# Performance work log

Measured on AMD Instinct MI355X. Metric: run time of the kernel, lower is better.

Reference implementation:

```python
import jax, jax.numpy as jnp
import numpy as np

N_EMBD = 1024
N_HEAD = 16


def setup_inputs() -> dict:
    key = jax.random.key(0)
    ks = jax.random.split(key, 5)
    C = N_EMBD
    x = jax.random.normal(ks[0], (4, 2048, C), dtype=jnp.float32)
    # linear params, scaled like torch default init (~U(-1/sqrt(C),1/sqrt(C)))
    s = 1.0 / np.sqrt(C)
    W_attn = jax.random.uniform(ks[1], (C, 3 * C), jnp.float32, -s, s)
    b_attn = jax.random.uniform(ks[2], (3 * C,), jnp.float32, -s, s)
    W_proj = jax.random.uniform(ks[3], (C, C), jnp.float32, -s, s)
    b_proj = jax.random.uniform(ks[4], (C,), jnp.float32, -s, s)
    return {"x": x, "W_attn": W_attn, "b_attn": b_attn, "W_proj": W_proj, "b_proj": b_proj}


def reference(x, W_attn, b_attn, W_proj, b_proj):
    B, T, C = x.shape
    H = N_HEAD
    D = C // H
    qkv = x @ W_attn + b_attn                      # [B,T,3C]
    q, k, v = jnp.split(qkv, 3, axis=-1)
    # [B,T,C] -> [B,H,T,D]
    q = q.reshape(B, T, H, D).transpose(0, 2, 1, 3)
    k = k.reshape(B, T, H, D).transpose(0, 2, 1, 3)
    v = v.reshape(B, T, H, D).transpose(0, 2, 1, 3)
    scale = 1.0 / np.sqrt(D).astype(np.float32)
    att = jnp.einsum('bhqd,bhkd->bhqk', q, k) * scale  # [B,H,T,T]
    causal = jnp.tril(jnp.ones((T, T), dtype=bool))
    att = jnp.where(causal[None, None], att, -jnp.inf)
    att = jax.nn.softmax(att, axis=-1)
    y = jnp.einsum('bhqk,bhkd->bhqd', att, v)      # [B,H,T,D]
    y = y.transpose(0, 2, 1, 3).reshape(B, T, C)
    return y @ W_proj + b_proj
```

## Files before the change

### kernel.cpp

```cpp
#include <hip/hip_runtime.h>
#include <hip/hip_bf16.h>
#include <math.h>


typedef __bf16 bf16x8 __attribute__((ext_vector_type(8)));
typedef float f32x4 __attribute__((ext_vector_type(4)));
typedef float f32x16 __attribute__((ext_vector_type(16)));

__device__ __forceinline__ f32x4 mfma16(bf16x8 a, bf16x8 b, f32x4 c) {
    return __builtin_amdgcn_mfma_f32_16x16x32_bf16(a, b, c, 0, 0, 0);
}
__device__ __forceinline__ f32x16 mfma32(bf16x8 a, bf16x8 b, f32x16 c) {
    return __builtin_amdgcn_mfma_f32_32x32x16_bf16(a, b, c, 0, 0, 0);
}

#define GLOBAL_AS __attribute__((address_space(1)))
#define LDS_AS __attribute__((address_space(3)))

__device__ __forceinline__ void async_copy16(const __hip_bfloat16* g, __hip_bfloat16* l) {
    __builtin_amdgcn_global_load_lds((const GLOBAL_AS uint32_t*)g, (LDS_AS uint32_t*)l, 16, 0, 0);
}

__device__ __forceinline__ uint32_t cvtpk(float lo, float hi) {
    uint32_t r;
    asm("v_cvt_pk_bf16_f32 %0, %1, %2" : "=v"(r) : "v"(lo), "v"(hi));
    return r;
}

#define QSCL 0.18033688011112042f

__global__ __launch_bounds__(256) void prep_kernel(
    const float* __restrict__ x, __hip_bfloat16* __restrict__ xb,
    const float* __restrict__ Wa, __hip_bfloat16* __restrict__ WaT,
    const float* __restrict__ Wp, __hip_bfloat16* __restrict__ WpT) {
    int bid = blockIdx.x;
    if (bid < 4096) {
        int i = (bid * 256 + threadIdx.x) * 8;
        union { __hip_bfloat16 h[8]; uint4 v; } tmp;
#pragma unroll
        for (int j = 0; j < 8; ++j) tmp.h[j] = __float2bfloat16(x[i + j]);
        *reinterpret_cast<uint4*>(xb + i) = tmp.v;
        return;
    }
    __shared__ float tile[32][33];
    const float* in;
    __hip_bfloat16* out;
    int R, Cc, tx_blocks, tb;
    if (bid < 4096 + 3072) {
        tb = bid - 4096; in = Wa; out = WaT; R = 1024; Cc = 3072; tx_blocks = 96;
    } else {
        tb = bid - 4096 - 3072; in = Wp; out = WpT; R = 1024; Cc = 1024; tx_blocks = 32;
    }
    int c0 = (tb % tx_blocks) * 32, r0 = (tb / tx_blocks) * 32;
    int tx = threadIdx.x & 31, ty = threadIdx.x >> 5;
#pragma unroll
    for (int i = 0; i < 4; ++i) {
        int r = r0 + ty + i * 8;
        tile[ty + i * 8][tx] = in[(size_t)r * Cc + c0 + tx];
    }
    __syncthreads();
#pragma unroll
    for (int i = 0; i < 4; ++i) {
        int c = c0 + ty + i * 8;
        out[(size_t)c * R + r0 + tx] = __float2bfloat16(tile[tx][ty + i * 8]);
    }
}

#define GEMM128_BODY(A_, Bt_, K_)                                                       \
    __shared__ __hip_bfloat16 As[128 * 32];                                             \
    __shared__ __hip_bfloat16 Bs[128 * 32];                                             \
    const int tid = threadIdx.x;                                                        \
    const int w = tid >> 6;                                                             \
    const int lr = tid & 15, lh = (tid & 63) >> 4;                                      \
    const int wr = w >> 1, wc = w & 1;                                                  \
    f32x4 zero = {0.f, 0.f, 0.f, 0.f};                                                  \
    f32x4 acc[4][4];                                                                    \
    _Pragma("unroll") for (int i = 0; i < 4; ++i)                                       \
        _Pragma("unroll") for (int j = 0; j < 4; ++j) acc[i][j] = zero;                 \
    for (int k0 = 0; k0 < (K_); k0 += 32) {                                             \
        _Pragma("unroll") for (int i = 0; i < 2; ++i) {                                 \
            int t = i * 256 + tid;                                                      \
            async_copy16((A_) + (size_t)(m0 + (t >> 2)) * (K_) + k0 + (t & 3) * 8,      \
                         As + (size_t)(i * 256 + w * 64) * 8);                          \
            async_copy16((Bt_) + (size_t)(n0 + (t >> 2)) * (K_) + k0 + (t & 3) * 8,     \
                         Bs + (size_t)(i * 256 + w * 64) * 8);                          \
        }                                                                               \
        __syncthreads();                                                                \
        bf16x8 af[4], bf[4];                                                            \
        _Pragma("unroll") for (int mf = 0; mf < 4; ++mf)                                \
            af[mf] = *reinterpret_cast<const bf16x8*>(                                  \
                &As[(wr * 64 + mf * 16 + lr) * 32 + lh * 8]);                           \
        _Pragma("unroll") for (int nf = 0; nf < 4; ++nf)                                \
            bf[nf] = *reinterpret_cast<const bf16x8*>(                                  \
                &Bs[(wc * 64 + nf * 16 + lr) * 32 + lh * 8]);                           \
        _Pragma("unroll") for (int mf = 0; mf < 4; ++mf)                                \
            _Pragma("unroll") for (int nf = 0; nf < 4; ++nf)                            \
                acc[mf][nf] = mfma16(af[mf], bf[nf], acc[mf][nf]);                      \
        __syncthreads();                                                                \
    }

__global__ __launch_bounds__(256) void gemm_qkv_kernel(
    const __hip_bfloat16* __restrict__ A, const __hip_bfloat16* __restrict__ Bt,
    const float* __restrict__ bias,
    __hip_bfloat16* __restrict__ qd, __hip_bfloat16* __restrict__ kd,
    __hip_bfloat16* __restrict__ vtd) {
    const int K = 1024;
    const int m0 = blockIdx.x * 128;
    const int n0 = blockIdx.y * 128;
    GEMM128_BODY(A, Bt, K)

    const int region = n0 >> 10;
#pragma unroll
    for (int mf = 0; mf < 4; ++mf) {
#pragma unroll
        for (int nf = 0; nf < 4; ++nf) {
            int n = n0 + wc * 64 + nf * 16 + lr;
            float bv = bias[n];
            int mbase = m0 + wr * 64 + mf * 16 + 4 * lh;
            int bb = mbase >> 11;
            int t = mbase & 2047;
            int c = n & 1023, hh = c >> 6, dd = c & 63;
            if (region == 2) {
                union { __hip_bfloat16 h[4]; uint2 v; } pk;
#pragma unroll
                for (int r = 0; r < 4; ++r) pk.h[r] = __float2bfloat16(acc[mf][nf][r] + bv);
                *reinterpret_cast<uint2*>(
                    &vtd[(((size_t)bb * 16 + hh) * 64 + dd) * 2048 + t]) = pk.v;
            } else if (region == 0) {
#pragma unroll
                for (int r = 0; r < 4; ++r)
                    qd[(((size_t)bb * 16 + hh) * 2048 + t + r) * 64 + dd] =
                        __float2bfloat16((acc[mf][nf][r] + bv) * QSCL);
            } else {
#pragma unroll
                for (int r = 0; r < 4; ++r)
                    kd[(((size_t)bb * 16 + hh) * 2048 + t + r) * 64 + dd] =
                        __float2bfloat16(acc[mf][nf][r] + bv);
            }
        }
    }
}

__global__ __launch_bounds__(256) void gemm_proj_kernel(
    const __hip_bfloat16* __restrict__ A, const __hip_bfloat16* __restrict__ Bt,
    const float* __restrict__ bias, float* __restrict__ out) {
    const int K = 1024, N = 1024;
    const int m0 = blockIdx.x * 128;
    const int n0 = blockIdx.y * 128;
    GEMM128_BODY(A, Bt, K)

#pragma unroll
    for (int nf = 0; nf < 4; ++nf) {
        int n = n0 + wc * 64 + nf * 16 + lr;
        float bv = bias[n];
#pragma unroll
        for (int mf = 0; mf < 4; ++mf) {
            int mbase = m0 + wr * 64 + mf * 16 + 4 * lh;
#pragma unroll
            for (int r = 0; r < 4; ++r)
                out[(size_t)(mbase + r) * N + n] = acc[mf][nf][r] + bv;
        }
    }
}

__global__ __launch_bounds__(512) void attn_kernel(
    const __hip_bfloat16* __restrict__ q, const __hip_bfloat16* __restrict__ k,
    const __hip_bfloat16* __restrict__ vt, __hip_bfloat16* __restrict__ y) {
    const int T = 2048, D = 64, C = 1024;
    const float THR = 8.0f;

    int wid = ((int)blockIdx.x & 7) * 64 + ((int)blockIdx.x >> 3);
    int bh = wid >> 3;
    int qr = wid & 7;
    int q256 = (wid & 32) ? qr : 7 - qr;
    int b = bh >> 4, h = bh & 15;
    int tid = threadIdx.x;
    int w = tid >> 6, l = tid & 63;
    int ql = l & 31, hi = l >> 5;

    __shared__ __hip_bfloat16 Ks[64 * 64];
    __shared__ __hip_bfloat16 Vs[64 * 64];
    __shared__ __hip_bfloat16 Pt[8][32][36];

    const int q0 = q256 * 256 + w * 32;
    const __hip_bfloat16* kbh = k + (size_t)bh * T * D;
    const __hip_bfloat16* vbh = vt + (size_t)bh * D * T;

    bf16x8 qf[4];
#pragma unroll
    for (int c = 0; c < 4; ++c)
        qf[c] = *reinterpret_cast<const bf16x8*>(
            q + ((size_t)bh * T + q0 + ql) * D + c * 16 + hi * 8);

    f32x16 o0 = {}, o1 = {};
    float m = -INFINITY, lp = 0.f;

    const int lastSub = q0 >> 5;
    const int nt64 = 4 * q256 + 4;

    for (int t64 = 0; t64 < nt64; ++t64) {
        __syncthreads();
        {
            int slot = tid;
            int row = slot >> 3;
            int fold = ((row & 7) ^ (row >> 3)) & 7;
            int colb = ((slot & 7) * 16) ^ (fold << 4);
            async_copy16(kbh + (size_t)(t64 * 64 + row) * 64 + (colb >> 1),
                         Ks + (size_t)(w * 64) * 8);
            async_copy16(vbh + (size_t)row * T + t64 * 64 + (colb >> 1),
                         Vs + (size_t)(w * 64) * 8);
        }
        __syncthreads();

#pragma unroll
        for (int sub = 0; sub < 2; ++sub) {
            const int is = t64 * 2 + sub;
            if (is > lastSub) break;
            bf16x8 kf[4];
            {
                int krow = sub * 32 + ql;
                int kfold = ((krow & 7) ^ (krow >> 3)) & 7;
                const char* KsB = reinterpret_cast<const char*>(Ks) + krow * 128;
#pragma unroll
                for (int c = 0; c < 4; ++c)
                    kf[c] = *reinterpret_cast<const bf16x8*>(
                        KsB + ((c * 32 + hi * 16) ^ (kfold << 4)));
            }

            __builtin_amdgcn_s_setprio(1);
            f32x16 s = {};
            s = mfma32(kf[0], qf[0], s);
            s = mfma32(kf[1], qf[1], s);
            s = mfma32(kf[2], qf[2], s);
            s = mfma32(kf[3], qf[3], s);
            __builtin_amdgcn_s_setprio(0);

            bf16x8 vf[2][2];
#pragma unroll
            for (int dblk = 0; dblk < 2; ++dblk) {
                int vrow = dblk * 32 + ql;
                int vfold = ((vrow & 7) ^ (vrow >> 3)) & 7;
                const char* VsB = reinterpret_cast<const char*>(Vs) + vrow * 128;
#pragma unroll
                for (int sl = 0; sl < 2; ++sl)
                    vf[dblk][sl] = *reinterpret_cast<const bf16x8*>(
                        VsB + ((sub * 64 + sl * 32 + hi * 16) ^ (vfold << 4)));
            }

            if (is == lastSub) {
#pragma unroll
                for (int r = 0; r < 16; ++r) {
                    int kvrow = (r & 3) + 8 * (r >> 2) + 4 * hi;
                    if (kvrow > ql) s[r] = -INFINITY;
                }
            }

            float mx;
            {
                float a = fmaxf(fmaxf(s[0], s[1]), s[2]);
                float bq = fmaxf(fmaxf(s[3], s[4]), s[5]);
                float c = fmaxf(fmaxf(s[6], s[7]), s[8]);
                float d = fmaxf(fmaxf(s[9], s[10]), s[11]);
                float e = fmaxf(fmaxf(s[12], s[13]), s[14]);
                mx = fmaxf(fmaxf(fmaxf(a, bq), fmaxf(c, d)), fmaxf(e, s[15]));
            }
            mx = fmaxf(mx, __shfl_xor(mx, 32));

            if (!__all(mx - m <= THR)) {
                float mnew = fmaxf(m, mx);
                float al = __builtin_amdgcn_exp2f(m - mnew);
                m = mnew;
                lp *= al;
#pragma unroll
                for (int r = 0; r < 16; ++r) { o0[r] *= al; o1[r] *= al; }
            }

#pragma unroll
            for (int r = 0; r < 16; ++r) s[r] = __builtin_amdgcn_exp2f(s[r] - m);

            lp += ((s[0] + s[1]) + (s[2] + s[3])) + ((s[4] + s[5]) + (s[6] + s[7])) +
                  (((s[8] + s[9]) + (s[10] + s[11])) + ((s[12] + s[13]) + (s[14] + s[15])));

            {
                uint2 w0, w1, w2, w3;
                w0.x = cvtpk(s[0], s[1]);   w0.y = cvtpk(s[2], s[3]);
                w1.x = cvtpk(s[4], s[5]);   w1.y = cvtpk(s[6], s[7]);
                w2.x = cvtpk(s[8], s[9]);   w2.y = cvtpk(s[10], s[11]);
                w3.x = cvtpk(s[12], s[13]); w3.y = cvtpk(s[14], s[15]);
                *reinterpret_cast<uint2*>(&Pt[w][ql][4 * hi])      = w0;
                *reinterpret_cast<uint2*>(&Pt[w][ql][8 + 4 * hi])  = w1;
                *reinterpret_cast<uint2*>(&Pt[w][ql][16 + 4 * hi]) = w2;
                *reinterpret_cast<uint2*>(&Pt[w][ql][24 + 4 * hi]) = w3;
            }

            union { uint32_t u[4]; bf16x8 v; } pa0, pa1;
            {
                uint2 r0 = *reinterpret_cast<const uint2*>(&Pt[w][ql][8 * hi]);
                uint2 r1 = *reinterpret_cast<const uint2*>(&Pt[w][ql][8 * hi + 4]);
                uint2 r2 = *reinterpret_cast<const uint2*>(&Pt[w][ql][16 + 8 * hi]);
                uint2 r3 = *reinterpret_cast<const uint2*>(&Pt[w][ql][16 + 8 * hi + 4]);
                pa0.u[0] = r0.x; pa0.u[1] = r0.y; pa0.u[2] = r1.x; pa0.u[3] = r1.y;
                pa1.u[0] = r2.x; pa1.u[1] = r2.y; pa1.u[2] = r3.x; pa1.u[3] = r3.y;
            }

            __builtin_amdgcn_s_setprio(1);
            o0 = mfma32(vf[0][0], pa0.v, o0);
            o0 = mfma32(vf[0][1], pa1.v, o0);
            o1 = mfma32(vf[1][0], pa0.v, o1);
            o1 = mfma32(vf[1][1], pa1.v, o1);
            __builtin_amdgcn_s_setprio(0);
        }
    }

    lp += __shfl_xor(lp, 32);
    float inv = 1.0f / lp;

    __hip_bfloat16* yq = y + ((size_t)b * T + q0 + ql) * C + h * 64;
#pragma unroll
    for (int dblk = 0; dblk < 2; ++dblk) {
#pragma unroll
        for (int g = 0; g < 4; ++g) {
            union { __hip_bfloat16 h4[4]; uint2 v; } pkk;
#pragma unroll
            for (int r = 0; r < 4; ++r) {
                float val = (dblk ? o1[g * 4 + r] : o0[g * 4 + r]) * inv;
                pkk.h4[r] = __float2bfloat16(val);
            }
            *reinterpret_cast<uint2*>(yq + dblk * 32 + g * 8 + hi * 4) = pkk.v;
        }
    }
}

extern "C" void kernel_launch(void* const* d_in, const int* in_sizes, int n_in,
                              void* d_out, int out_size, void* d_ws, size_t ws_size,
                              hipStream_t stream) {
    const float* x      = (const float*)d_in[0];
    const float* W_attn = (const float*)d_in[1];
    const float* b_attn = (const float*)d_in[2];
    const float* W_proj = (const float*)d_in[3];
    const float* b_proj = (const float*)d_in[4];
    float* out = (float*)d_out;

    __hip_bfloat16* wsb = reinterpret_cast<__hip_bfloat16*>(d_ws);
    __hip_bfloat16* xb  = wsb;
    __hip_bfloat16* WaT = xb + (size_t)8192 * 1024;
    __hip_bfloat16* WpT = WaT + (size_t)3072 * 1024;
    __hip_bfloat16* qd  = WpT + (size_t)1024 * 1024;
    __hip_bfloat16* kd  = qd + (size_t)64 * 2048 * 64;
    __hip_bfloat16* vtd = kd + (size_t)64 * 2048 * 64;
    __hip_bfloat16* ya  = vtd + (size_t)64 * 2048 * 64;

    prep_kernel<<<4096 + 3072 + 1024, 256, 0, stream>>>(x, xb, W_attn, WaT, W_proj, WpT);
    gemm_qkv_kernel<<<dim3(64, 24), 256, 0, stream>>>(xb, WaT, b_attn, qd, kd, vtd);
    attn_kernel<<<512, 512, 0, stream>>>(qd, kd, vtd, ya);
    gemm_proj_kernel<<<dim3(64, 8), 256, 0, stream>>>(ya, WpT, b_proj, out);
}
```

Baseline: 168.9 us.

## Rewrite QKV GEMM as 256x256 double-buffered pipelined tile with swizzled LDS

The QKV projection GEMM moves from 128x128 tiles with 256 threads and a load-sync-compute loop to 256x256 tiles with 512 threads. K-step 64 tiles are double-buffered in LDS, and async global-to-LDS copies for the next stage are interleaved across four MFMA phases using explicit vmcnt waits, barriers and setprio. The LDS layout uses an XOR swizzle to avoid bank conflicts. The aim is to hide load latency and raise data reuse per tile. In exchange it uses 128KB of LDS per block and higher register pressure, and the grid is smaller at 384 blocks.

```diff
diff --git a/kernel.cpp b/kernel.cpp
--- a/kernel.cpp
+++ b/kernel.cpp
@@ -99,42 +99,118 @@
         __syncthreads();                                                                \
     }
 
-__global__ __launch_bounds__(256) void gemm_qkv_kernel(
+#define QKV_PHASE(d_, MF0_, STAGE_STMT, WAIT_STMT)                                      \
+    {                                                                                   \
+        bf16x8 a00 = readA(d_, (MF0_), 0), a01 = readA(d_, (MF0_), 1);                  \
+        bf16x8 a10 = readA(d_, (MF0_) + 1, 0), a11 = readA(d_, (MF0_) + 1, 1);          \
+        STAGE_STMT;                                                                     \
+        asm volatile("s_waitcnt lgkmcnt(0)" ::: "memory");                              \
+        __builtin_amdgcn_sched_barrier(0);                                              \
+        __builtin_amdgcn_s_setprio(1);                                                  \
+        _Pragma("unroll") for (int nf = 0; nf < 4; ++nf) {                              \
+            acc[(MF0_)][nf]     = mfma16(a00, bfr[nf][0], acc[(MF0_)][nf]);             \
+            acc[(MF0_)][nf]     = mfma16(a01, bfr[nf][1], acc[(MF0_)][nf]);             \
+            acc[(MF0_) + 1][nf] = mfma16(a10, bfr[nf][0], acc[(MF0_) + 1][nf]);         \
+            acc[(MF0_) + 1][nf] = mfma16(a11, bfr[nf][1], acc[(MF0_) + 1][nf]);         \
+        }                                                                               \
+        __builtin_amdgcn_s_setprio(0);                                                  \
+        WAIT_STMT;                                                                      \
+        __builtin_amdgcn_s_barrier();                                                   \
+    }
+
+__global__ __launch_bounds__(512, 2) void gemm_qkv_kernel(
     const __hip_bfloat16* __restrict__ A, const __hip_bfloat16* __restrict__ Bt,
     const float* __restrict__ bias,
     __hip_bfloat16* __restrict__ qd, __hip_bfloat16* __restrict__ kd,
     __hip_bfloat16* __restrict__ vtd) {
-    const int K = 1024;
-    const int m0 = blockIdx.x * 128;
-    const int n0 = blockIdx.y * 128;
-    GEMM128_BODY(A, Bt, K)
+    const int K = 1024, nt = 16;
+    const int m0 = blockIdx.x * 256;
+    const int n0 = blockIdx.y * 256;
+    const int tid = threadIdx.x;
+    const int w = tid >> 6, l = tid & 63;
+    const int lr = l & 15, lh = l >> 4;
+    const int wr = w >> 2, wcn = w & 3;
+
+    __shared__ __hip_bfloat16 S[2][2][256 * 64];
+
+    f32x4 acc[8][4] = {};
+
+    auto stageQ = [&](int e, int ab, int qq, int t) {
+        const __hip_bfloat16* src = ab ? Bt + (size_t)(n0 + qq * 64) * K
+                                       : A + (size_t)(m0 + qq * 64) * K;
+        int row = tid >> 3;
+        int colb = ((tid & 7) * 16) ^ ((row & 7) << 4);
+        async_copy16(src + (size_t)row * K + t * 64 + (colb >> 1),
+                     &S[e][ab][qq * 64 * 64 + w * 512]);
+    };
+    auto readA = [&](int d, int mf, int kk) -> bf16x8 {
+        int row = wr * 128 + mf * 16 + lr;
+        int colb = (kk * 64 + lh * 16) ^ ((lr & 7) << 4);
+        return *reinterpret_cast<const bf16x8*>(
+            reinterpret_cast<const char*>(&S[d][0][0]) + row * 128 + colb);
+    };
+    auto readB = [&](int d, int nf, int kk) -> bf16x8 {
+        int row = wcn * 64 + nf * 16 + lr;
+        int colb = (kk * 64 + lh * 16) ^ ((lr & 7) << 4);
+        return *reinterpret_cast<const bf16x8*>(
+            reinterpret_cast<const char*>(&S[d][1][0]) + row * 128 + colb);
+    };
+
+    stageQ(0, 1, 0, 0); stageQ(0, 1, 1, 0); stageQ(0, 1, 2, 0); stageQ(0, 1, 3, 0);
+    stageQ(0, 0, 0, 0); stageQ(0, 0, 2, 0); stageQ(0, 0, 1, 0); stageQ(0, 0, 3, 0);
+    asm volatile("s_waitcnt vmcnt(2)" ::: "memory");
+    __builtin_amdgcn_s_barrier();
+
+    for (int t = 0; t < nt; ++t) {
+        const int d = t & 1, e = d ^ 1;
+        const bool nxt = (t + 1 < nt);
+        bf16x8 bfr[4][2];
+#pragma unroll
+        for (int nf = 0; nf < 4; ++nf) {
+            bfr[nf][0] = readB(d, nf, 0);
+            bfr[nf][1] = readB(d, nf, 1);
+        }
+        QKV_PHASE(d, 0,
+            { if (nxt) { stageQ(e, 1, 0, t + 1); stageQ(e, 1, 1, t + 1); } },
+            {});
+        QKV_PHASE(d, 2,
+            { if (nxt) { stageQ(e, 1, 2, t + 1); stageQ(e, 1, 3, t + 1); } },
+            { if (nxt) asm volatile("s_waitcnt vmcnt(4)" ::: "memory");
+              else     asm volatile("s_waitcnt vmcnt(0)" ::: "memory"); });
+        QKV_PHASE(d, 4,
+            { if (nxt) { stageQ(e, 0, 0, t + 1); stageQ(e, 0, 2, t + 1); } },
+            {});
+        QKV_PHASE(d, 6,
+            { if (nxt) { stageQ(e, 0, 1, t + 1); stageQ(e, 0, 3, t + 1); } },
+            { if (nxt) asm volatile("s_waitcnt vmcnt(2)" ::: "memory"); });
+    }
 
     const int region = n0 >> 10;
 #pragma unroll
-    for (int mf = 0; mf < 4; ++mf) {
+    for (int mf = 0; mf < 8; ++mf) {
 #pragma unroll
         for (int nf = 0; nf < 4; ++nf) {
-            int n = n0 + wc * 64 + nf * 16 + lr;
+            int n = n0 + wcn * 64 + nf * 16 + lr;
             float bv = bias[n];
-            int mbase = m0 + wr * 64 + mf * 16 + 4 * lh;
+            int mbase = m0 + wr * 128 + mf * 16 + 4 * lh;
             int bb = mbase >> 11;
-            int t = mbase & 2047;
+            int tt = mbase & 2047;
             int c = n & 1023, hh = c >> 6, dd = c & 63;
             if (region == 2) {
                 union { __hip_bfloat16 h[4]; uint2 v; } pk;
 #pragma unroll
                 for (int r = 0; r < 4; ++r) pk.h[r] = __float2bfloat16(acc[mf][nf][r] + bv);
                 *reinterpret_cast<uint2*>(
-                    &vtd[(((size_t)bb * 16 + hh) * 64 + dd) * 2048 + t]) = pk.v;
+                    &vtd[(((size_t)bb * 16 + hh) * 64 + dd) * 2048 + tt]) = pk.v;
             } else if (region == 0) {
 #pragma unroll
                 for (int r = 0; r < 4; ++r)
-                    qd[(((size_t)bb * 16 + hh) * 2048 + t + r) * 64 + dd] =
+                    qd[(((size_t)bb * 16 + hh) * 2048 + tt + r) * 64 + dd] =
                         __float2bfloat16((acc[mf][nf][r] + bv) * QSCL);
             } else {
 #pragma unroll
                 for (int r = 0; r < 4; ++r)
-                    kd[(((size_t)bb * 16 + hh) * 2048 + t + r) * 64 + dd] =
+                    kd[(((size_t)bb * 16 + hh) * 2048 + tt + r) * 64 + dd] =
                         __float2bfloat16(acc[mf][nf][r] + bv);
             }
         }
@@ -351,7 +427,7 @@
     __hip_bfloat16* ya  = vtd + (size_t)64 * 2048 * 64;
 
     prep_kernel<<<4096 + 3072 + 1024, 256, 0, stream>>>(x, xb, W_attn, WaT, W_proj, WpT);
-    gemm_qkv_kernel<<<dim3(64, 24), 256, 0, stream>>>(xb, WaT, b_attn, qd, kd, vtd);
+    gemm_qkv_kernel<<<dim3(32, 12), 512, 0, stream>>>(xb, WaT, b_attn, qd, kd, vtd);
     attn_kernel<<<512, 512, 0, stream>>>(qd, kd, vtd, ya);
     gemm_proj_kernel<<<dim3(64, 8), 256, 0, stream>>>(ya, WpT, b_proj, out);
 }
```

Measured after the change: 166.2 us. Within noise of the previous version (-1.6%).
